# Performance work log

Measured on AMD Instinct MI355X. Metric: run time of the kernel, lower is better.

Reference implementation:

```python
import jax, jax.numpy as jnp
import numpy as np

Nu, Ni, Nb, Nc, Nr = 100000, 100000, 5000, 2000, 50000
E, Eb, Ec, Er = 600000, 100000, 200000, 400000
D, L = 64, 50


def _seg_softmax(logits, seg, n):
    m = jax.ops.segment_max(logits, seg, num_segments=n)
    e = jnp.exp(logits - m[seg])
    s = jax.ops.segment_sum(e, seg, num_segments=n)
    return e / (s[seg] + 1e-9)


def setup_inputs():
    key = jax.random.key(0)
    ks = jax.random.split(key, 32)
    f = lambda i, shape, s=0.05: jax.random.normal(ks[i], shape, jnp.float32) * s
    return dict(
        user_h=f(0, (Nu, D), 1.0), item_h=f(1, (Ni, D), 1.0),
        brand_feat=f(2, (Nb, D), 1.0), cat_feat=f(3, (Nc, D), 1.0), rel_feat=f(4, (Nr, D), 1.0),
        Wu=f(5, (D, D)), Wi=f(6, (D, D)), Wb=f(7, (D, D)), Wc=f(8, (D, D)), Wr=f(9, (D, D)),
        Wg_u=f(10, (2 * D, D)), Wg_i=f(11, (2 * D, D)),
        u_pos=f(12, (L, D)), u_pos_k=f(13, (L, D)), i_pos=f(14, (L, D)), i_pos_k=f(15, (L, D)),
        basis_freq=jnp.asarray(1.0 / 10 ** np.linspace(0, 9, D), jnp.float32),
        phase=jnp.zeros((D,), jnp.float32),
        Wr0=f(16, (D, D)), Wr1=f(17, (D, D)), Wr2=f(18, (D, D)),
        e_time=jax.random.uniform(ks[19], (E,), jnp.float32),
        e_iid=jax.random.randint(ks[20], (E,), 0, Ni),
        e_uid=jax.random.randint(ks[21], (E,), 0, Nu),
        pos_u=jax.random.randint(ks[22], (E,), 0, L),
        pos_i=jax.random.randint(ks[23], (E,), 0, L),
        eb_src=jax.random.randint(ks[24], (Eb,), 0, Nb),
        eb_dst=jax.random.randint(ks[25], (Eb,), 0, Ni),
        ec_src=jax.random.randint(ks[26], (Ec,), 0, Nc),
        ec_dst=jax.random.randint(ks[27], (Ec,), 0, Ni),
        er_src=jax.random.randint(ks[28], (Er,), 0, Nr),
        er_dst=jax.random.randint(ks[29], (Er,), 0, Ni),
    )


def reference(user_h, item_h, brand_feat, cat_feat, rel_feat, Wu, Wi, Wb, Wc, Wr,
              Wg_u, Wg_i, u_pos, u_pos_k, i_pos, i_pos_k, basis_freq, phase,
              Wr0, Wr1, Wr2, e_time,
              e_iid, e_uid, pos_u, pos_i, eb_src, eb_dst, ec_src, ec_dst, er_src, er_dst):
    sqrtD = jnp.sqrt(jnp.float32(D))
    # relation-specific linear transforms (user_weight / item_weight / att_trans)
    uh = user_h @ Wu                      # [Nu,D]
    ih = item_h @ Wi                      # [Ni,D]
    bf = brand_feat @ Wb
    cf = cat_feat @ Wc
    rf = rel_feat @ Wr
    # TimeEncode harmonic features per purchase edge
    t_enc = jnp.cos(e_time[:, None] * basis_freq[None, :] + phase[None, :])  # [E,D]

    hi = ih[e_iid]                        # [E,D] item-side gather
    hu = uh[e_uid]                        # [E,D] user-side gather

    # ---- user aggregation: 'orgat' long-term (pos + time aware) + 'att' short-term ----
    k_long = hi + u_pos_k[pos_u] + t_enc
    a_long = _seg_softmax(jnp.sum(k_long * hu, -1) / sqrtD, e_uid, Nu)
    h_long_u = jax.ops.segment_sum(a_long[:, None] * (hi + u_pos[pos_u]), e_uid, num_segments=Nu)
    a_short = _seg_softmax(jnp.sum(hi * hu, -1) / sqrtD, e_uid, Nu)
    h_short_u = jax.ops.segment_sum(a_short[:, None] * hi, e_uid, num_segments=Nu)
    user_new = jnp.concatenate([h_long_u, h_short_u], -1) @ Wg_u  # agg_gate_u

    # ---- item aggregation from users (symmetric) ----
    k_long_i = hu + i_pos_k[pos_i] + t_enc
    b_long = _seg_softmax(jnp.sum(k_long_i * hi, -1) / sqrtD, e_iid, Ni)
    h_long_i = jax.ops.segment_sum(b_long[:, None] * (hu + i_pos[pos_i]), e_iid, num_segments=Ni)
    b_short = _seg_softmax(jnp.sum(hu * hi, -1) / sqrtD, e_iid, Ni)
    h_short_i = jax.ops.segment_sum(b_short[:, None] * hu, e_iid, num_segments=Ni)
    item_new = jnp.concatenate([h_long_i, h_short_i], -1) @ Wg_i  # agg_gate_i

    # ---- relation mean aggregation onto items (reduce_trans per relation) ----
    def mean_agg(feat, src, dst, W):
        s = jax.ops.segment_sum(feat[src], dst, num_segments=Ni)
        c = jax.ops.segment_sum(jnp.ones(src.shape, feat.dtype), dst, num_segments=Ni)
        return (s / jnp.maximum(c, 1.0)[:, None]) @ W

    item_new = item_new + mean_agg(bf, eb_src, eb_dst, Wr0) \
                        + mean_agg(cf, ec_src, ec_dst, Wr1) \
                        + mean_agg(rf, er_src, er_dst, Wr2)

    # residual update: elu(now + old)
    user_out = jax.nn.elu(user_new + user_h)
    item_out = jax.nn.elu(item_new + item_h)
    return user_out, item_out
```

## Files before the change

kernel.cpp:

```cpp
#include <hip/hip_runtime.h>
#include <hip/hip_bf16.h>
#include <hip/hip_fp16.h>

typedef __hip_bfloat16 bf16_t;

#define NU 100000
#define NI 100000
#define NB_ 5000
#define NC_ 2000
#define NR_ 50000
#define NE 600000
#define NEB 100000
#define NEC 200000
#define NER 400000
#define NPERM (2 * NE + NEB + NEC + NER)
#define NRELE (NEB + NEC + NER)
#define NALL (NE + NRELE)
#define SCAN_N (2 * NU + NI + 1)
#define SCAN_CHUNK 2048
#define SCAN_NCHUNK ((SCAN_N + SCAN_CHUNK - 1) / SCAN_CHUNK)
#define PBLK 4096
#define RBLK ((NRELE + 255) / 256)

typedef __attribute__((ext_vector_type(8))) short short8;
typedef __attribute__((ext_vector_type(4))) short short4v;
typedef __attribute__((ext_vector_type(4))) float f32x4;

__device__ __forceinline__ float b2f(bf16_t x) { return __bfloat162float(x); }
__device__ __forceinline__ float sane(float x) { return isfinite(x) ? x : 0.f; }
__device__ __forceinline__ unsigned short f2bu(float x) {
    union { bf16_t b; unsigned short u; } c; c.b = __float2bfloat16(x); return c.u;
}

__device__ __forceinline__ float ldf(const void* p, size_t i, int f32) {
    return f32 ? ((const float*)p)[i] : __bfloat162float(((const bf16_t*)p)[i]);
}
__device__ __forceinline__ void stf(void* p, size_t i, float v, int f32) {
    if (f32) ((float*)p)[i] = v;
    else     ((bf16_t*)p)[i] = __float2bfloat16(v);
}

__device__ __forceinline__ f32x4 bf4(const bf16_t* p) {
    short4v s = *(const short4v*)p;
    f32x4 r;
#pragma unroll
    for (int q = 0; q < 4; ++q)
        r[q] = __uint_as_float(((unsigned)(unsigned short)s[q]) << 16);
    return r;
}
__device__ __forceinline__ f32x4 ldf4(const void* p, size_t i, int f32) {
    if (f32) return *(const f32x4*)((const float*)p + i);
    return bf4((const bf16_t*)p + i);
}

__device__ __forceinline__ void bf8(const bf16_t* p, float* o) {
    short8 s = *(const short8*)p;
#pragma unroll
    for (int q = 0; q < 8; ++q)
        o[q] = __uint_as_float(((unsigned)(unsigned short)s[q]) << 16);
}
__device__ __forceinline__ void ldf8(const void* p, size_t i, int f32, float* o) {
    if (f32) {
        f32x4 a = *(const f32x4*)((const float*)p + i);
        f32x4 b = *(const f32x4*)((const float*)p + i + 4);
#pragma unroll
        for (int q = 0; q < 4; ++q) { o[q] = a[q]; o[4 + q] = b[q]; }
    } else {
        bf8((const bf16_t*)p + i, o);
    }
}

__global__ void detect_dtype(const unsigned int* w, int* flag) {
    if (threadIdx.x == 0 && blockIdx.x == 0) *flag = (w[0] == 0x3F800000u) ? 1 : 0;
}

__global__ __launch_bounds__(256) void combine_w(
    const void* Wb, const void* Wr0,
    const void* Wc, const void* Wr1,
    const void* Wr, const void* Wr2,
    bf16_t* out, const int* flagp) {
    int f = *flagp;
    int mat = blockIdx.x >> 4;
    int sub = blockIdx.x & 15;
    const void* A = mat == 0 ? Wb : (mat == 1 ? Wc : Wr);
    const void* B = mat == 0 ? Wr0 : (mat == 1 ? Wr1 : Wr2);
    int idx = sub * 256 + threadIdx.x;
    int i = idx >> 6, j = idx & 63;
    float acc = 0.f;
    for (int k = 0; k < 64; ++k)
        acc = fmaf(ldf(A, i * 64 + k, f), ldf(B, k * 64 + j, f), acc);
    out[(size_t)mat * 4096 + idx] = __float2bfloat16(acc);
}

struct GSeg {
    const void* A; const void* W; void* out;
    const void* hext; const bf16_t* relb;
    int M; int orow0; int out_mode; int a_internal; int w_internal;
};

__global__ __launch_bounds__(256) void gemm_multi(
    GSeg s0, GSeg s1, GSeg s2, GSeg s3, GSeg s4,
    int nseg, int K, const int* __restrict__ flagp) {
    __shared__ short WL[128 * 64];
    int f = *flagp;
    int nt0 = (s0.M + 63) >> 6;
    int nt1 = (nseg > 1) ? ((s1.M + 63) >> 6) : 0;
    int nt2 = (nseg > 2) ? ((s2.M + 63) >> 6) : 0;
    int nt3 = (nseg > 3) ? ((s3.M + 63) >> 6) : 0;
    int nt4 = (nseg > 4) ? ((s4.M + 63) >> 6) : 0;
    int c0 = nt0, c1 = c0 + nt1, c2 = c1 + nt2, c3 = c2 + nt3;
    int ntT = c3 + nt4;
    int lane = threadIdx.x & 63;
    int wv = threadIdx.x >> 6;
    int q = lane >> 4, nl = lane & 15;
    int KK = K >> 5;
    int staged = -1;
    for (int tile = blockIdx.x; tile < ntT; tile += gridDim.x) {
        int sidx, t_in;
        if (tile < c0) { sidx = 0; t_in = tile; }
        else if (tile < c1) { sidx = 1; t_in = tile - c0; }
        else if (tile < c2) { sidx = 2; t_in = tile - c1; }
        else if (tile < c3) { sidx = 3; t_in = tile - c2; }
        else { sidx = 4; t_in = tile - c3; }
        const void* A; const void* W; void* out; const void* hext; const bf16_t* relb;
        int M, orow0, out_mode, a_int, w_int;
        if (sidx == 0) {
            A = s0.A; W = s0.W; out = s0.out; hext = s0.hext; relb = s0.relb;
            M = s0.M; orow0 = s0.orow0; out_mode = s0.out_mode; a_int = s0.a_internal; w_int = s0.w_internal;
        } else if (sidx == 1) {
            A = s1.A; W = s1.W; out = s1.out; hext = s1.hext; relb = s1.relb;
            M = s1.M; orow0 = s1.orow0; out_mode = s1.out_mode; a_int = s1.a_internal; w_int = s1.w_internal;
        } else if (sidx == 2) {
            A = s2.A; W = s2.W; out = s2.out; hext = s2.hext; relb = s2.relb;
            M = s2.M; orow0 = s2.orow0; out_mode = s2.out_mode; a_int = s2.a_internal; w_int = s2.w_internal;
        } else if (sidx == 3) {
            A = s3.A; W = s3.W; out = s3.out; hext = s3.hext; relb = s3.relb;
            M = s3.M; orow0 = s3.orow0; out_mode = s3.out_mode; a_int = s3.a_internal; w_int = s3.w_internal;
        } else {
            A = s4.A; W = s4.W; out = s4.out; hext = s4.hext; relb = s4.relb;
            M = s4.M; orow0 = s4.orow0; out_mode = s4.out_mode; a_int = s4.a_internal; w_int = s4.w_internal;
        }
        if (sidx != staged) {
            __syncthreads();
            int w_f32 = w_int ? 0 : f;
            for (int i = threadIdx.x; i < K * 64; i += 256) {
                int j = i & 7, ln = (i >> 3) & 63, p = i >> 9;
                int kk4 = p >> 2, n0t = p & 3;
                int srow = kk4 * 32 + (ln >> 4) * 8 + j;
                int scol = n0t * 16 + (ln & 15);
                float wvv = w_f32 ? ((const float*)W)[srow * 64 + scol]
                                  : b2f(((const bf16_t*)W)[srow * 64 + scol]);
                WL[i] = (short)f2bu(wvv);
            }
            __syncthreads();
            staged = sidx;
        }
        int m0 = t_in * 64 + wv * 16;
        if (m0 < M) {
            int a_f32 = a_int ? 0 : f;
            int arow = m0 + nl; if (arow >= M) arow = M - 1;
            f32x4 acc[4];
#pragma unroll
            for (int t = 0; t < 4; ++t) acc[t] = (f32x4){0.f, 0.f, 0.f, 0.f};
            for (int kk4 = 0; kk4 < KK; ++kk4) {
                short8 af;
                size_t abase = (size_t)arow * K + kk4 * 32 + q * 8;
                if (a_f32) {
                    const f32x4* ap = (const f32x4*)((const float*)A + abase);
                    f32x4 x0 = ap[0], x1 = ap[1];
#pragma unroll
                    for (int j = 0; j < 4; ++j) {
                        af[j] = (short)f2bu(x0[j]);
                        af[4 + j] = (short)f2bu(x1[j]);
                    }
                } else {
                    af = *(const short8*)((const bf16_t*)A + abase);
                }
#pragma unroll
                for (int n0t = 0; n0t < 4; ++n0t) {
                    short8 bfr = *(const short8*)&WL[(((kk4 << 2) + n0t) * 64 + lane) * 8];
                    acc[n0t] = __builtin_amdgcn_mfma_f32_16x16x32_bf16(af, bfr, acc[n0t], 0, 0, 0);
                }
            }
#pragma unroll
            for (int n0t = 0; n0t < 4; ++n0t) {
#pragma unroll
                for (int r = 0; r < 4; ++r) {
                    int row = m0 + q * 4 + r;
                    if (row >= M) continue;
                    int col = n0t * 16 + nl;
                    float v = acc[n0t][r];
                    if (out_mode == 1) {
                        v += ldf(hext, (size_t)row * 64 + col, f);
                        if (relb) v += b2f(relb[(size_t)row * 64 + col]);
                        v = v > 0.f ? v : expm1f(v);
                        stf(out, (size_t)(row + orow0) * 64 + col, sane(v), f);
                    } else {
                        ((bf16_t*)out)[(size_t)row * 64 + col] = __float2bfloat16(v);
                    }
                }
            }
        }
    }
}

__global__ __launch_bounds__(256) void hist_all(
    const int* __restrict__ e_uid, const int* __restrict__ e_iid,
    const int* __restrict__ eb_dst, const int* __restrict__ ec_dst,
    const int* __restrict__ er_dst, int* __restrict__ deg) {
    int t = blockIdx.x * blockDim.x + threadIdx.x;
    if (t < NE) {
        atomicAdd(deg + e_uid[t], 1);
        atomicAdd(deg + NU + e_iid[t], 1);
    } else if (t < NE + NEB) {
        atomicAdd(deg + 2 * NU + eb_dst[t - NE], 1);
    } else if (t < NE + NEB + NEC) {
        atomicAdd(deg + 2 * NU + ec_dst[t - NE - NEB], 1);
    } else if (t < NALL) {
        atomicAdd(deg + 2 * NU + er_dst[t - NE - NEB - NEC], 1);
    }
}

__global__ __launch_bounds__(256) void scan1(const int* __restrict__ deg,
                                             int* __restrict__ off,
                                             int* __restrict__ ctot) {
    __shared__ int part[256];
    int base = blockIdx.x * SCAN_CHUNK + threadIdx.x * 8;
    int v[8]; int s = 0;
#pragma unroll
    for (int k = 0; k < 8; ++k) {
        int idx = base + k;
        v[k] = s;
        s += (idx < SCAN_N) ? deg[idx] : 0;
    }
    part[threadIdx.x] = s;
    __syncthreads();
    for (int o = 1; o < 256; o <<= 1) {
        int t = (threadIdx.x >= o) ? part[threadIdx.x - o] : 0;
        __syncthreads();
        part[threadIdx.x] += t;
        __syncthreads();
    }
    int texc = (threadIdx.x == 0) ? 0 : part[threadIdx.x - 1];
#pragma unroll
    for (int k = 0; k < 8; ++k) {
        int idx = base + k;
        if (idx < SCAN_N) off[idx] = texc + v[k];
    }
    if (threadIdx.x == 255) ctot[blockIdx.x] = part[255];
}
__global__ __launch_bounds__(256) void scan23(int* __restrict__ off,
                                              const int* __restrict__ ctot,
                                              int* __restrict__ cur) {
    __shared__ int part[256];
    int t = threadIdx.x;
    part[t] = (t < SCAN_NCHUNK) ? ctot[t] : 0;
    __syncthreads();
    for (int o = 1; o < 256; o <<= 1) {
        int x = (t >= o) ? part[t - o] : 0;
        __syncthreads();
        part[t] += x;
        __syncthreads();
    }
    int add = blockIdx.x ? part[blockIdx.x - 1] : 0;
    int base = blockIdx.x * SCAN_CHUNK + t;
#pragma unroll
    for (int k = 0; k < 8; ++k) {
        int idx = base + k * 256;
        if (idx < SCAN_N) { int v = off[idx] + add; off[idx] = v; cur[idx] = v; }
    }
}

__global__ __launch_bounds__(256) void edges_fused(
    const bf16_t* __restrict__ uh, const bf16_t* __restrict__ ih,
    const void* __restrict__ u_pos_k, const void* __restrict__ i_pos_k,
    const void* __restrict__ basis_freq, const void* __restrict__ phase_,
    const void* __restrict__ e_time,
    const int* __restrict__ e_uid, const int* __restrict__ e_iid,
    const int* __restrict__ pos_u, const int* __restrict__ pos_i,
    const int* __restrict__ eb_src, const int* __restrict__ eb_dst,
    const int* __restrict__ ec_src, const int* __restrict__ ec_dst,
    const int* __restrict__ er_src, const int* __restrict__ er_dst,
    int* __restrict__ cur, uint2* __restrict__ perm, const int* flagp) {
    if (blockIdx.x >= PBLK) {
        int t = (blockIdx.x - PBLK) * 256 + threadIdx.x;
        if (t < NEB) {
            int p = atomicAdd(cur + 2 * NU + eb_dst[t], 1);
            perm[p] = make_uint2((unsigned)eb_src[t], 0u);
        } else if (t < NEB + NEC) {
            int e = t - NEB;
            int p = atomicAdd(cur + 2 * NU + ec_dst[e], 1);
            perm[p] = make_uint2((unsigned)(ec_src[e] + NB_) | (1u << 17), 0u);
        } else if (t < NRELE) {
            int e = t - NEB - NEC;
            int p = atomicAdd(cur + 2 * NU + er_dst[e], 1);
            perm[p] = make_uint2((unsigned)(er_src[e] + NB_ + NC_) | (2u << 17), 0u);
        }
        return;
    }
    int f = *flagp;
    int lane = threadIdx.x & 63;
    int g = lane >> 3, l = lane & 7;
    float bfv[8], phv[8];
    ldf8(basis_freq, (size_t)l * 8, f, bfv);
    ldf8(phase_, (size_t)l * 8, f, phv);
    int w = (blockIdx.x * 256 + threadIdx.x) >> 6;
    const int NWAVE = PBLK * 4;
    for (int eb = w; eb < NE / 8; eb += NWAVE) {
        int e = eb * 8 + g;
        int uid = e_uid[e], iid = e_iid[e], pu = pos_u[e], pi = pos_i[e];
        float t = ldf(e_time, e, f);
        float hu[8], hi[8], pku[8], pki[8];
        bf8(uh + (size_t)uid * 64 + l * 8, hu);
        bf8(ih + (size_t)iid * 64 + l * 8, hi);
        ldf8(u_pos_k, (size_t)pu * 64 + l * 8, f, pku);
        ldf8(i_pos_k, (size_t)pi * 64 + l * 8, f, pki);
        float d_lu = 0.f, d_sh = 0.f, d_li = 0.f;
#pragma unroll
        for (int qq = 0; qq < 8; ++qq) {
            float te = __cosf(fmaf(t, bfv[qq], phv[qq]));
            d_lu = fmaf(hi[qq] + pku[qq] + te, hu[qq], d_lu);
            d_sh = fmaf(hi[qq], hu[qq], d_sh);
            d_li = fmaf(hu[qq] + pki[qq] + te, hi[qq], d_li);
        }
#pragma unroll
        for (int o = 1; o < 8; o <<= 1) {
            d_lu += __shfl_xor(d_lu, o, 64);
            d_sh += __shfl_xor(d_sh, o, 64);
            d_li += __shfl_xor(d_li, o, 64);
        }
        if (l == 0) {
            float p_lu = __expf(fminf(d_lu * 0.125f, 10.f));
            float p_sh = __expf(fminf(d_sh * 0.125f, 10.f));
            float p_li = __expf(fminf(d_li * 0.125f, 10.f));
            unsigned pkt_u = (unsigned)__half_as_ushort(__float2half(p_lu))
                           | ((unsigned)__half_as_ushort(__float2half(p_sh)) << 16);
            unsigned pkt_i = (unsigned)__half_as_ushort(__float2half(p_li))
                           | ((unsigned)__half_as_ushort(__float2half(p_sh)) << 16);
            int s1 = atomicAdd(cur + uid, 1);
            perm[s1] = make_uint2((unsigned)iid | ((unsigned)pu << 17), pkt_u);
            int s2 = atomicAdd(cur + NU + iid, 1);
            perm[s2] = make_uint2((unsigned)uid | ((unsigned)pi << 17), pkt_i);
        }
    }
}

__global__ __launch_bounds__(256) void gather_all(
    const bf16_t* __restrict__ uh, const bf16_t* __restrict__ ih,
    const void* __restrict__ u_pos, const void* __restrict__ i_pos,
    const int* __restrict__ off, const uint2* __restrict__ perm,
    const bf16_t* __restrict__ fW,
    bf16_t* __restrict__ aggU, bf16_t* __restrict__ aggI,
    bf16_t* __restrict__ relb, const int* flagp) {
    int f = *flagp;
    int lane = threadIdx.x & 63;
    int l = lane & 15;
    int gb = lane & 48;
    int l4 = l * 4;
    int v = blockIdx.x * 16 + (threadIdx.x >> 4);
    int phase = v >= NU;
    int vtx = phase ? v - NU : v;
    const bf16_t* other = phase ? uh : ih;
    const void* pv = phase ? i_pos : u_pos;
    int j0 = off[v], j1 = off[v + 1];
    f32x4 a0 = (f32x4){0.f, 0.f, 0.f, 0.f}, a1 = a0;
    float s1 = 0.f, s2 = 0.f;
    for (int cb = j0; cb < j1; cb += 16) {
        int m = j1 - cb; if (m > 16) m = 16;
        uint2 pay = make_uint2(0u, 0u);
        if (l < m) pay = perm[cb + l];
        unsigned px0 = (unsigned)__shfl((int)pay.x, gb, 64);
        unsigned py0 = (unsigned)__shfl((int)pay.y, gb, 64);
        f32x4 ho0 = bf4(other + (size_t)(px0 & 0x1FFFF) * 64 + l4);
        f32x4 pv0 = ldf4(pv, (size_t)((px0 >> 17) & 63) * 64 + l4, f);
        for (int k = 0; k < m; ++k) {
            unsigned px1 = 0, py1 = 0;
            f32x4 ho1 = (f32x4){0.f, 0.f, 0.f, 0.f}, pv1 = ho1;
            if (k + 1 < m) {
                px1 = (unsigned)__shfl((int)pay.x, gb + k + 1, 64);
                py1 = (unsigned)__shfl((int)pay.y, gb + k + 1, 64);
                ho1 = bf4(other + (size_t)(px1 & 0x1FFFF) * 64 + l4);
                pv1 = ldf4(pv, (size_t)((px1 >> 17) & 63) * 64 + l4, f);
            }
            float p1 = __half2float(__ushort_as_half((unsigned short)(py0 & 0xFFFF)));
            float p2 = __half2float(__ushort_as_half((unsigned short)(py0 >> 16)));
#pragma unroll
            for (int q = 0; q < 4; ++q) {
                a0[q] = fmaf(p1, ho0[q] + pv0[q], a0[q]);
                a1[q] = fmaf(p2, ho0[q], a1[q]);
            }
            s1 += p1; s2 += p2;
            px0 = px1; py0 = py1; ho0 = ho1; pv0 = pv1;
        }
    }
    float inv1 = 1.f / (s1 + 1e-9f), inv2 = 1.f / (s2 + 1e-9f);
    bf16_t* aggRow = (phase ? aggI : aggU) + (size_t)vtx * 128;
    short4v o0, o1;
#pragma unroll
    for (int q = 0; q < 4; ++q) {
        o0[q] = (short)f2bu(a0[q] * inv1);
        o1[q] = (short)f2bu(a1[q] * inv2);
    }
    *(short4v*)(aggRow + l4) = o0;
    *(short4v*)(aggRow + 64 + l4) = o1;
    if (phase) {
        f32x4 r0 = (f32x4){0.f, 0.f, 0.f, 0.f}, r1 = r0, r2 = r0;
        int c0 = 0, c1 = 0, c2 = 0;
        int k0 = off[2 * NU + vtx], k1 = off[2 * NU + vtx + 1];
        for (int cb = k0; cb < k1; cb += 16) {
            int m = k1 - cb; if (m > 16) m = 16;
            unsigned px = 0u;
            if (l < m) px = perm[cb + l].x;
            unsigned u0 = (unsigned)__shfl((int)px, gb, 64);
            f32x4 fv0 = bf4(fW + (size_t)(u0 & 0x1FFFF) * 64 + l4);
            for (int k = 0; k < m; ++k) {
                unsigned u1 = 0;
                f32x4 fv1 = (f32x4){0.f, 0.f, 0.f, 0.f};
                if (k + 1 < m) {
                    u1 = (unsigned)__shfl((int)px, gb + k + 1, 64);
                    fv1 = bf4(fW + (size_t)(u1 & 0x1FFFF) * 64 + l4);
                }
                int r = (u0 >> 17) & 3;
                if (r == 0) {
#pragma unroll
                    for (int q = 0; q < 4; ++q) r0[q] += fv0[q];
                    c0++;
                } else if (r == 1) {
#pragma unroll
                    for (int q = 0; q < 4; ++q) r1[q] += fv0[q];
                    c1++;
                } else {
#pragma unroll
                    for (int q = 0; q < 4; ++q) r2[q] += fv0[q];
                    c2++;
                }
                u0 = u1; fv0 = fv1;
            }
        }
        float w0 = 1.f / fmaxf((float)c0, 1.f);
        float w1 = 1.f / fmaxf((float)c1, 1.f);
        float w2 = 1.f / fmaxf((float)c2, 1.f);
        short4v ro;
#pragma unroll
        for (int q = 0; q < 4; ++q)
            ro[q] = (short)f2bu(r0[q] * w0 + r1[q] * w1 + r2[q] * w2);
        *(short4v*)(relb + (size_t)vtx * 64 + l4) = ro;
    }
}

extern "C" void kernel_launch(void* const* d_in, const int* in_sizes, int n_in,
                              void* d_out, int out_size, void* d_ws, size_t ws_size,
                              hipStream_t stream) {
    const void* user_h     = d_in[0];
    const void* item_h     = d_in[1];
    const void* brand_feat = d_in[2];
    const void* cat_feat   = d_in[3];
    const void* rel_feat   = d_in[4];
    const void* Wu   = d_in[5];
    const void* Wi   = d_in[6];
    const void* Wb   = d_in[7];
    const void* Wc   = d_in[8];
    const void* Wr   = d_in[9];
    const void* Wg_u = d_in[10];
    const void* Wg_i = d_in[11];
    const void* u_pos   = d_in[12];
    const void* u_pos_k = d_in[13];
    const void* i_pos   = d_in[14];
    const void* i_pos_k = d_in[15];
    const void* basis_freq = d_in[16];
    const void* phase      = d_in[17];
    const void* Wr0 = d_in[18];
    const void* Wr1 = d_in[19];
    const void* Wr2 = d_in[20];
    const void* e_time = d_in[21];
    const int* e_iid  = (const int*)d_in[22];
    const int* e_uid  = (const int*)d_in[23];
    const int* pos_u  = (const int*)d_in[24];
    const int* pos_i  = (const int*)d_in[25];
    const int* eb_src = (const int*)d_in[26];
    const int* eb_dst = (const int*)d_in[27];
    const int* ec_src = (const int*)d_in[28];
    const int* ec_dst = (const int*)d_in[29];
    const int* er_src = (const int*)d_in[30];
    const int* er_dst = (const int*)d_in[31];

    char* base = (char*)d_ws;
    size_t off_b = 0;
    auto alloc = [&](size_t bytes) { size_t p = off_b; off_b = (off_b + bytes + 511) & ~(size_t)511; return p; };
    size_t o_flag  = alloc(512);
    size_t o_uh    = alloc((size_t)NU * 64 * 2);
    size_t o_ih    = alloc((size_t)NI * 64 * 2);
    size_t o_fW    = alloc((size_t)(NB_ + NC_ + NR_ + 64) * 64 * 2);
    size_t o_wcomb = alloc((size_t)3 * 4096 * 2);
    size_t o_deg   = alloc((size_t)SCAN_N * 4);
    size_t o_off   = alloc((size_t)SCAN_N * 4);
    size_t o_cur   = alloc((size_t)SCAN_N * 4);
    size_t o_ctot  = alloc((size_t)SCAN_NCHUNK * 4);
    size_t o_perm  = alloc((size_t)NPERM * 8);
    size_t o_aggU  = alloc((size_t)(NU + 64) * 128 * 2);
    size_t o_aggI  = alloc((size_t)(NI + 64) * 128 * 2);
    size_t o_relb  = alloc((size_t)(NI + 64) * 64 * 2);

    int*    flagp = (int*)(base + o_flag);
    bf16_t* uh    = (bf16_t*)(base + o_uh);
    bf16_t* ih    = (bf16_t*)(base + o_ih);
    bf16_t* fW    = (bf16_t*)(base + o_fW);
    bf16_t* wcomb = (bf16_t*)(base + o_wcomb);
    int*    deg   = (int*)(base + o_deg);
    int*    offp  = (int*)(base + o_off);
    int*    cur   = (int*)(base + o_cur);
    int*    ctot  = (int*)(base + o_ctot);
    uint2*  perm  = (uint2*)(base + o_perm);
    bf16_t* aggU  = (bf16_t*)(base + o_aggU);
    bf16_t* aggI  = (bf16_t*)(base + o_aggI);
    bf16_t* relb  = (bf16_t*)(base + o_relb);

    hipMemsetAsync(deg, 0, (size_t)SCAN_N * 4, stream);
    detect_dtype<<<1, 64, 0, stream>>>((const unsigned int*)basis_freq, flagp);

    combine_w<<<48, 256, 0, stream>>>(Wb, Wr0, Wc, Wr1, Wr, Wr2, wcomb, flagp);

    {
        GSeg su = {user_h,     Wu,           uh,                            nullptr, nullptr, NU,  0, 0, 0, 0};
        GSeg si = {item_h,     Wi,           ih,                            nullptr, nullptr, NI,  0, 0, 0, 0};
        GSeg sb = {brand_feat, wcomb,        fW,                            nullptr, nullptr, NB_, 0, 0, 0, 1};
        GSeg sc = {cat_feat,   wcomb + 4096, fW + (size_t)NB_ * 64,         nullptr, nullptr, NC_, 0, 0, 0, 1};
        GSeg sr = {rel_feat,   wcomb + 8192, fW + (size_t)(NB_ + NC_) * 64, nullptr, nullptr, NR_, 0, 0, 0, 1};
        gemm_multi<<<1024, 256, 0, stream>>>(su, si, sb, sc, sr, 5, 64, flagp);
    }

    hist_all<<<(NALL + 255) / 256, 256, 0, stream>>>(e_uid, e_iid, eb_dst, ec_dst, er_dst, deg);
    scan1<<<SCAN_NCHUNK, 256, 0, stream>>>(deg, offp, ctot);
    scan23<<<SCAN_NCHUNK, 256, 0, stream>>>(offp, ctot, cur);

    edges_fused<<<PBLK + RBLK, 256, 0, stream>>>(uh, ih, u_pos_k, i_pos_k, basis_freq, phase,
                                                 e_time, e_uid, e_iid, pos_u, pos_i,
                                                 eb_src, eb_dst, ec_src, ec_dst,
                                                 er_src, er_dst, cur, perm, flagp);

    gather_all<<<(NU + NI) / 16, 256, 0, stream>>>(uh, ih, u_pos, i_pos, offp, perm, fW,
                                                   aggU, aggI, relb, flagp);

    {
        GSeg su = {aggU, Wg_u, d_out, user_h, nullptr, NU, 0,  1, 1, 0};
        GSeg si = {aggI, Wg_i, d_out, item_h, relb,    NI, NU, 1, 1, 0};
        gemm_multi<<<512, 256, 0, stream>>>(su, si, su, su, su, 2, 128, flagp);
    }
}
```

Baseline: 573.5 us.

## Fuse gate GEMM and ELU epilogue into the gather kernel

The gather kernel now keeps each block's 16 aggregated rows (and the relation-mean row) in shared memory and applies the gate matrix with MFMA right there, then adds the residual, applies ELU and writes the final output. This removes the aggU/aggI/relb round-trip through global memory and one kernel launch. The gate weights are pre-swizzled by the combine kernel. The edge kernel also spreads the two atomic scatter writes across two lanes, and PBLK is doubled. In exchange, each gather block carries more work and shared memory plus a barrier.

```diff
diff --git a/kernel.cpp b/kernel.cpp
--- a/kernel.cpp
+++ b/kernel.cpp
@@ -19,8 +19,11 @@
 #define SCAN_N (2 * NU + NI + 1)
 #define SCAN_CHUNK 2048
 #define SCAN_NCHUNK ((SCAN_N + SCAN_CHUNK - 1) / SCAN_CHUNK)
-#define PBLK 4096
+#define PBLK 8192
 #define RBLK ((NRELE + 255) / 256)
+
+#define AGS 136
+#define RLS 68
 
 typedef __attribute__((ext_vector_type(8))) short short8;
 typedef __attribute__((ext_vector_type(4))) short short4v;
@@ -78,30 +81,43 @@
     const void* Wb, const void* Wr0,
     const void* Wc, const void* Wr1,
     const void* Wr, const void* Wr2,
-    bf16_t* out, const int* flagp) {
+    const void* Wg_u, const void* Wg_i,
+    bf16_t* out, bf16_t* wgsw, const int* flagp) {
     int f = *flagp;
-    int mat = blockIdx.x >> 4;
-    int sub = blockIdx.x & 15;
-    const void* A = mat == 0 ? Wb : (mat == 1 ? Wc : Wr);
-    const void* B = mat == 0 ? Wr0 : (mat == 1 ? Wr1 : Wr2);
-    int idx = sub * 256 + threadIdx.x;
-    int i = idx >> 6, j = idx & 63;
-    float acc = 0.f;
-    for (int k = 0; k < 64; ++k)
-        acc = fmaf(ldf(A, i * 64 + k, f), ldf(B, k * 64 + j, f), acc);
-    out[(size_t)mat * 4096 + idx] = __float2bfloat16(acc);
+    if (blockIdx.x < 48) {
+        int mat = blockIdx.x >> 4;
+        int sub = blockIdx.x & 15;
+        const void* A = mat == 0 ? Wb : (mat == 1 ? Wc : Wr);
+        const void* B = mat == 0 ? Wr0 : (mat == 1 ? Wr1 : Wr2);
+        int idx = sub * 256 + threadIdx.x;
+        int i = idx >> 6, j = idx & 63;
+        float acc = 0.f;
+        for (int k = 0; k < 64; ++k)
+            acc = fmaf(ldf(A, i * 64 + k, f), ldf(B, k * 64 + j, f), acc);
+        out[(size_t)mat * 4096 + idx] = __float2bfloat16(acc);
+    } else {
+        int t = (blockIdx.x - 48) * 256 + threadIdx.x;
+        int mat = t >> 13;
+        int i = t & 8191;
+        int j = i & 7, ln = (i >> 3) & 63, p = i >> 9;
+        int kk4 = p >> 2, n0t = p & 3;
+        int srow = kk4 * 32 + (ln >> 4) * 8 + j;
+        int scol = n0t * 16 + (ln & 15);
+        const void* src = mat ? Wg_i : Wg_u;
+        wgsw[(size_t)mat * 8192 + i] = __float2bfloat16(ldf(src, (size_t)srow * 64 + scol, f));
+    }
 }
 
 struct GSeg {
     const void* A; const void* W; void* out;
-    const void* hext; const bf16_t* relb;
-    int M; int orow0; int out_mode; int a_internal; int w_internal;
+    int M; int a_internal; int w_internal;
 };
 
 __global__ __launch_bounds__(256) void gemm_multi(
     GSeg s0, GSeg s1, GSeg s2, GSeg s3, GSeg s4,
-    int nseg, int K, const int* __restrict__ flagp) {
-    __shared__ short WL[128 * 64];
+    int nseg, const int* __restrict__ flagp) {
+    const int K = 64;
+    __shared__ short WL[64 * 64];
     int f = *flagp;
     int nt0 = (s0.M + 63) >> 6;
     int nt1 = (nseg > 1) ? ((s1.M + 63) >> 6) : 0;
@@ -113,7 +129,6 @@
     int lane = threadIdx.x & 63;
     int wv = threadIdx.x >> 6;
     int q = lane >> 4, nl = lane & 15;
-    int KK = K >> 5;
     int staged = -1;
     for (int tile = blockIdx.x; tile < ntT; tile += gridDim.x) {
         int sidx, t_in;
@@ -122,24 +137,12 @@
         else if (tile < c2) { sidx = 2; t_in = tile - c1; }
         else if (tile < c3) { sidx = 3; t_in = tile - c2; }
         else { sidx = 4; t_in = tile - c3; }
-        const void* A; const void* W; void* out; const void* hext; const bf16_t* relb;
-        int M, orow0, out_mode, a_int, w_int;
-        if (sidx == 0) {
-            A = s0.A; W = s0.W; out = s0.out; hext = s0.hext; relb = s0.relb;
-            M = s0.M; orow0 = s0.orow0; out_mode = s0.out_mode; a_int = s0.a_internal; w_int = s0.w_internal;
-        } else if (sidx == 1) {
-            A = s1.A; W = s1.W; out = s1.out; hext = s1.hext; relb = s1.relb;
-            M = s1.M; orow0 = s1.orow0; out_mode = s1.out_mode; a_int = s1.a_internal; w_int = s1.w_internal;
-        } else if (sidx == 2) {
-            A = s2.A; W = s2.W; out = s2.out; hext = s2.hext; relb = s2.relb;
-            M = s2.M; orow0 = s2.orow0; out_mode = s2.out_mode; a_int = s2.a_internal; w_int = s2.w_internal;
-        } else if (sidx == 3) {
-            A = s3.A; W = s3.W; out = s3.out; hext = s3.hext; relb = s3.relb;
-            M = s3.M; orow0 = s3.orow0; out_mode = s3.out_mode; a_int = s3.a_internal; w_int = s3.w_internal;
-        } else {
-            A = s4.A; W = s4.W; out = s4.out; hext = s4.hext; relb = s4.relb;
-            M = s4.M; orow0 = s4.orow0; out_mode = s4.out_mode; a_int = s4.a_internal; w_int = s4.w_internal;
-        }
+        const void* A; const void* W; void* out; int M, a_int, w_int;
+        if (sidx == 0)      { A = s0.A; W = s0.W; out = s0.out; M = s0.M; a_int = s0.a_internal; w_int = s0.w_internal; }
+        else if (sidx == 1) { A = s1.A; W = s1.W; out = s1.out; M = s1.M; a_int = s1.a_internal; w_int = s1.w_internal; }
+        else if (sidx == 2) { A = s2.A; W = s2.W; out = s2.out; M = s2.M; a_int = s2.a_internal; w_int = s2.w_internal; }
+        else if (sidx == 3) { A = s3.A; W = s3.W; out = s3.out; M = s3.M; a_int = s3.a_internal; w_int = s3.w_internal; }
+        else                { A = s4.A; W = s4.W; out = s4.out; M = s4.M; a_int = s4.a_internal; w_int = s4.w_internal; }
         if (sidx != staged) {
             __syncthreads();
             int w_f32 = w_int ? 0 : f;
@@ -162,7 +165,7 @@
             f32x4 acc[4];
 #pragma unroll
             for (int t = 0; t < 4; ++t) acc[t] = (f32x4){0.f, 0.f, 0.f, 0.f};
-            for (int kk4 = 0; kk4 < KK; ++kk4) {
+            for (int kk4 = 0; kk4 < 2; ++kk4) {
                 short8 af;
                 size_t abase = (size_t)arow * K + kk4 * 32 + q * 8;
                 if (a_f32) {
@@ -189,15 +192,7 @@
                     int row = m0 + q * 4 + r;
                     if (row >= M) continue;
                     int col = n0t * 16 + nl;
-                    float v = acc[n0t][r];
-                    if (out_mode == 1) {
-                        v += ldf(hext, (size_t)row * 64 + col, f);
-                        if (relb) v += b2f(relb[(size_t)row * 64 + col]);
-                        v = v > 0.f ? v : expm1f(v);
-                        stf(out, (size_t)(row + orow0) * 64 + col, sane(v), f);
-                    } else {
-                        ((bf16_t*)out)[(size_t)row * 64 + col] = __float2bfloat16(v);
-                    }
+                    ((bf16_t*)out)[(size_t)row * 64 + col] = __float2bfloat16(acc[n0t][r]);
                 }
             }
         }
@@ -332,32 +327,38 @@
         if (l == 0) {
             float p_lu = __expf(fminf(d_lu * 0.125f, 10.f));
             float p_sh = __expf(fminf(d_sh * 0.125f, 10.f));
-            float p_li = __expf(fminf(d_li * 0.125f, 10.f));
             unsigned pkt_u = (unsigned)__half_as_ushort(__float2half(p_lu))
-                           | ((unsigned)__half_as_ushort(__float2half(p_sh)) << 16);
-            unsigned pkt_i = (unsigned)__half_as_ushort(__float2half(p_li))
                            | ((unsigned)__half_as_ushort(__float2half(p_sh)) << 16);
             int s1 = atomicAdd(cur + uid, 1);
             perm[s1] = make_uint2((unsigned)iid | ((unsigned)pu << 17), pkt_u);
+        } else if (l == 1) {
+            float p_li = __expf(fminf(d_li * 0.125f, 10.f));
+            float p_sh = __expf(fminf(d_sh * 0.125f, 10.f));
+            unsigned pkt_i = (unsigned)__half_as_ushort(__float2half(p_li))
+                           | ((unsigned)__half_as_ushort(__float2half(p_sh)) << 16);
             int s2 = atomicAdd(cur + NU + iid, 1);
             perm[s2] = make_uint2((unsigned)uid | ((unsigned)pi << 17), pkt_i);
         }
     }
 }
 
-__global__ __launch_bounds__(256) void gather_all(
+__global__ __launch_bounds__(256) void gather_gemm(
     const bf16_t* __restrict__ uh, const bf16_t* __restrict__ ih,
     const void* __restrict__ u_pos, const void* __restrict__ i_pos,
     const int* __restrict__ off, const uint2* __restrict__ perm,
-    const bf16_t* __restrict__ fW,
-    bf16_t* __restrict__ aggU, bf16_t* __restrict__ aggI,
-    bf16_t* __restrict__ relb, const int* flagp) {
+    const bf16_t* __restrict__ fW, const bf16_t* __restrict__ wgsw,
+    const void* __restrict__ user_h, const void* __restrict__ item_h,
+    void* __restrict__ d_out, const int* flagp) {
+    __shared__ short AG[16 * AGS];
+    __shared__ short RL[16 * RLS];
     int f = *flagp;
     int lane = threadIdx.x & 63;
     int l = lane & 15;
     int gb = lane & 48;
     int l4 = l * 4;
-    int v = blockIdx.x * 16 + (threadIdx.x >> 4);
+    int grp = threadIdx.x >> 4;
+    int v0 = blockIdx.x * 16;
+    int v = v0 + grp;
     int phase = v >= NU;
     int vtx = phase ? v - NU : v;
     const bf16_t* other = phase ? uh : ih;
@@ -394,15 +395,16 @@
         }
     }
     float inv1 = 1.f / (s1 + 1e-9f), inv2 = 1.f / (s2 + 1e-9f);
-    bf16_t* aggRow = (phase ? aggI : aggU) + (size_t)vtx * 128;
-    short4v o0, o1;
-#pragma unroll
-    for (int q = 0; q < 4; ++q) {
-        o0[q] = (short)f2bu(a0[q] * inv1);
-        o1[q] = (short)f2bu(a1[q] * inv2);
-    }
-    *(short4v*)(aggRow + l4) = o0;
-    *(short4v*)(aggRow + 64 + l4) = o1;
+    {
+        short4v o0, o1;
+#pragma unroll
+        for (int q = 0; q < 4; ++q) {
+            o0[q] = (short)f2bu(a0[q] * inv1);
+            o1[q] = (short)f2bu(a1[q] * inv2);
+        }
+        *(short4v*)&AG[grp * AGS + l4] = o0;
+        *(short4v*)&AG[grp * AGS + 64 + l4] = o1;
+    }
     if (phase) {
         f32x4 r0 = (f32x4){0.f, 0.f, 0.f, 0.f}, r1 = r0, r2 = r0;
         int c0 = 0, c1 = 0, c2 = 0;
@@ -444,7 +446,30 @@
 #pragma unroll
         for (int q = 0; q < 4; ++q)
             ro[q] = (short)f2bu(r0[q] * w0 + r1[q] * w1 + r2[q] * w2);
-        *(short4v*)(relb + (size_t)vtx * 64 + l4) = ro;
+        *(short4v*)&RL[grp * RLS + l4] = ro;
+    }
+    __syncthreads();
+    int wv = threadIdx.x >> 6;
+    int q = lane >> 4, nl = lane & 15;
+    const bf16_t* wg = wgsw + (phase ? 8192 : 0);
+    f32x4 acc = (f32x4){0.f, 0.f, 0.f, 0.f};
+#pragma unroll
+    for (int kk = 0; kk < 4; ++kk) {
+        short8 af = *(const short8*)&AG[nl * AGS + kk * 32 + q * 8];
+        short8 bfr = *(const short8*)&wg[(((kk << 2) + wv) * 64 + lane) * 8];
+        acc = __builtin_amdgcn_mfma_f32_16x16x32_bf16(af, bfr, acc, 0, 0, 0);
+    }
+    const void* hext = phase ? item_h : user_h;
+    int hbase = phase ? v0 - NU : v0;
+#pragma unroll
+    for (int r = 0; r < 4; ++r) {
+        int row = q * 4 + r;
+        int col = wv * 16 + nl;
+        float val = acc[r];
+        val += ldf(hext, (size_t)(hbase + row) * 64 + col, f);
+        if (phase) val += b2f(((const bf16_t*)RL)[row * RLS + col]);
+        val = val > 0.f ? val : expm1f(val);
+        stf(d_out, (size_t)(v0 + row) * 64 + col, sane(val), f);
     }
 }
 
@@ -492,41 +517,38 @@
     size_t o_ih    = alloc((size_t)NI * 64 * 2);
     size_t o_fW    = alloc((size_t)(NB_ + NC_ + NR_ + 64) * 64 * 2);
     size_t o_wcomb = alloc((size_t)3 * 4096 * 2);
+    size_t o_wgsw  = alloc((size_t)2 * 8192 * 2);
     size_t o_deg   = alloc((size_t)SCAN_N * 4);
     size_t o_off   = alloc((size_t)SCAN_N * 4);
     size_t o_cur   = alloc((size_t)SCAN_N * 4);
     size_t o_ctot  = alloc((size_t)SCAN_NCHUNK * 4);
     size_t o_perm  = alloc((size_t)NPERM * 8);
-    size_t o_aggU  = alloc((size_t)(NU + 64) * 128 * 2);
-    size_t o_aggI  = alloc((size_t)(NI + 64) * 128 * 2);
-    size_t o_relb  = alloc((size_t)(NI + 64) * 64 * 2);
 
     int*    flagp = (int*)(base + o_flag);
     bf16_t* uh    = (bf16_t*)(base + o_uh);
     bf16_t* ih    = (bf16_t*)(base + o_ih);
     bf16_t* fW    = (bf16_t*)(base + o_fW);
     bf16_t* wcomb = (bf16_t*)(base + o_wcomb);
+    bf16_t* wgsw  = (bf16_t*)(base + o_wgsw);
     int*    deg   = (int*)(base + o_deg);
     int*    offp  = (int*)(base + o_off);
     int*    cur   = (int*)(base + o_cur);
     int*    ctot  = (int*)(base + o_ctot);
     uint2*  perm  = (uint2*)(base + o_perm);
-    bf16_t* aggU  = (bf16_t*)(base + o_aggU);
-    bf16_t* aggI  = (bf16_t*)(base + o_aggI);
-    bf16_t* relb  = (bf16_t*)(base + o_relb);
 
     hipMemsetAsync(deg, 0, (size_t)SCAN_N * 4, stream);
     detect_dtype<<<1, 64, 0, stream>>>((const unsigned int*)basis_freq, flagp);
 
-    combine_w<<<48, 256, 0, stream>>>(Wb, Wr0, Wc, Wr1, Wr, Wr2, wcomb, flagp);
+    combine_w<<<112, 256, 0, stream>>>(Wb, Wr0, Wc, Wr1, Wr, Wr2, Wg_u, Wg_i,
+                                       wcomb, wgsw, flagp);
 
     {
-        GSeg su = {user_h,     Wu,           uh,                            nullptr, nullptr, NU,  0, 0, 0, 0};
-        GSeg si = {item_h,     Wi,           ih,                            nullptr, nullptr, NI,  0, 0, 0, 0};
-        GSeg sb = {brand_feat, wcomb,        fW,                            nullptr, nullptr, NB_, 0, 0, 0, 1};
-        GSeg sc = {cat_feat,   wcomb + 4096, fW + (size_t)NB_ * 64,         nullptr, nullptr, NC_, 0, 0, 0, 1};
-        GSeg sr = {rel_feat,   wcomb + 8192, fW + (size_t)(NB_ + NC_) * 64, nullptr, nullptr, NR_, 0, 0, 0, 1};
-        gemm_multi<<<1024, 256, 0, stream>>>(su, si, sb, sc, sr, 5, 64, flagp);
+        GSeg su = {user_h,     Wu,           uh,                            NU,  0, 0};
+        GSeg si = {item_h,     Wi,           ih,                            NI,  0, 0};
+        GSeg sb = {brand_feat, wcomb,        fW,                            NB_, 0, 1};
+        GSeg sc = {cat_feat,   wcomb + 4096, fW + (size_t)NB_ * 64,         NC_, 0, 1};
+        GSeg sr = {rel_feat,   wcomb + 8192, fW + (size_t)(NB_ + NC_) * 64, NR_, 0, 1};
+        gemm_multi<<<1024, 256, 0, stream>>>(su, si, sb, sc, sr, 5, flagp);
     }
 
     hist_all<<<(NALL + 255) / 256, 256, 0, stream>>>(e_uid, e_iid, eb_dst, ec_dst, er_dst, deg);
@@ -538,12 +560,6 @@
                                                  eb_src, eb_dst, ec_src, ec_dst,
                                                  er_src, er_dst, cur, perm, flagp);
 
-    gather_all<<<(NU + NI) / 16, 256, 0, stream>>>(uh, ih, u_pos, i_pos, offp, perm, fW,
-                                                   aggU, aggI, relb, flagp);
-
-    {
-        GSeg su = {aggU, Wg_u, d_out, user_h, nullptr, NU, 0,  1, 1, 0};
-        GSeg si = {aggI, Wg_i, d_out, item_h, relb,    NI, NU, 1, 1, 0};
-        gemm_multi<<<512, 256, 0, stream>>>(su, si, su, su, su, 2, 128, flagp);
-    }
-}
+    gather_gemm<<<(NU + NI) / 16, 256, 0, stream>>>(uh, ih, u_pos, i_pos, offp, perm, fW,
+                                                    wgsw, user_h, item_h, d_out, flagp);
+}
```

New measurement: 514.2 us. 10.3% less time.
